# Kernel optimization log

Measured on AMD Instinct MI355X. Metric: run time of the kernel, lower is better.

Reference implementation:

```python
import jax, jax.numpy as jnp
import numpy as np

B, C, H, W = 8, 64, 128, 128
OC, KH, KW = 64, 3, 3
STRIDE, PAD, DIL = 1, 1, 1
DG = 1            # deformable groups
G = 1             # conv groups
K = KH * KW
HO = (H + 2 * PAD - DIL * (KH - 1) - 1) // STRIDE + 1
WO = (W + 2 * PAD - DIL * (KW - 1) - 1) // STRIDE + 1


def setup_inputs() -> dict:
    key = jax.random.key(0)
    k1, k2, k3, k4 = jax.random.split(key, 4)
    input_tensor = jax.random.normal(k1, (B, C, H, W), dtype=jnp.float32)
    offset = jax.random.normal(k2, (B, DG * 2 * K, HO, WO), dtype=jnp.float32)
    mask = jax.random.uniform(k3, (B, DG * K, HO, WO), dtype=jnp.float32)
    n = C * KH * KW
    std_v = 1.0 / np.sqrt(n)
    weight = jax.random.uniform(k4, (OC, C // G, KH, KW), dtype=jnp.float32,
                                minval=-std_v, maxval=std_v)
    bias = jnp.zeros((OC,), dtype=jnp.float32)
    return {"input_tensor": input_tensor, "offset": offset, "mask": mask,
            "weight": weight, "bias": bias}


def _bilinear_sample(img, py, px):
    # img: [Cg, H, W]; py, px: [K, HO, WO] fractional sample coords
    y0 = jnp.floor(py).astype(jnp.int32)
    x0 = jnp.floor(px).astype(jnp.int32)
    y1, x1 = y0 + 1, x0 + 1
    wy1 = py - y0.astype(py.dtype)
    wx1 = px - x0.astype(px.dtype)
    wy0, wx0 = 1.0 - wy1, 1.0 - wx1

    def gather(yy, xx):
        valid = ((yy >= 0) & (yy < H) & (xx >= 0) & (xx < W)).astype(img.dtype)
        yc = jnp.clip(yy, 0, H - 1)
        xc = jnp.clip(xx, 0, W - 1)
        return img[:, yc, xc] * valid  # [Cg, K, HO, WO], zero outside

    return (gather(y0, x0) * (wy0 * wx0) + gather(y0, x1) * (wy0 * wx1)
            + gather(y1, x0) * (wy1 * wx0) + gather(y1, x1) * (wy1 * wx1))


def _mdconv(input_tensor, offset, mask, weight, bias):
    Cg = C // DG
    ky = (jnp.arange(K) // KW).astype(jnp.float32)   # kernel row per tap
    kx = (jnp.arange(K) % KW).astype(jnp.float32)    # kernel col per tap
    oy = jnp.arange(HO, dtype=jnp.float32) * STRIDE - PAD
    ox = jnp.arange(WO, dtype=jnp.float32) * STRIDE - PAD
    base_y = ky[:, None] * DIL + oy[None, :]         # [K, HO]
    base_x = kx[:, None] * DIL + ox[None, :]         # [K, WO]

    off = offset.reshape(B, DG, K, 2, HO, WO)
    py = base_y[None, None, :, :, None] + off[:, :, :, 0]  # [B, DG, K, HO, WO]
    px = base_x[None, None, :, None, :] + off[:, :, :, 1]

    imgs = input_tensor.reshape(B, DG, Cg, H, W)
    sample = jax.vmap(jax.vmap(_bilinear_sample))           # over B then DG
    cols = sample(imgs, py, px)                             # [B, DG, Cg, K, HO, WO]
    cols = cols * mask.reshape(B, DG, 1, K, HO, WO)
    cols = cols.reshape(B, G, C // G, K, HO, WO)

    w = weight.reshape(G, OC // G, C // G, K)
    out = jnp.einsum('gock,bgckpq->bgopq', w, cols)
    out = out.reshape(B, OC, HO, WO) + bias[None, :, None, None]
    return out


def reference(input_tensor, offset, mask, weight, bias):
    return _mdconv(input_tensor, offset, mask, weight, bias)
```

## Files before the change

### kernel.cpp

```cpp
#include <hip/hip_runtime.h>
#include <stdint.h>

typedef unsigned short u16;

#define B_ 8
#define C_ 64
#define H_ 128
#define W_ 128
#define OC_ 64
#define HO_ 128
#define WO_ 128
#define HWC_ (H_*W_*C_)
#define PADW 72

typedef __attribute__((ext_vector_type(8))) _Float16 f16x8;
typedef __attribute__((ext_vector_type(2))) _Float16 h2;
typedef __attribute__((ext_vector_type(4))) float f32x4;

__device__ __forceinline__ u16 f2h(float f) {
  union { _Float16 h; u16 u; } c; c.h = (_Float16)f; return c.u;
}
__device__ __forceinline__ uint32_t pkh2(float f) {
  union { _Float16 h[2]; uint32_t u; } c;
  const _Float16 h = (_Float16)f;
  c.h[0] = h; c.h[1] = h; return c.u;
}

__global__ void wprep_kernel(const float* __restrict__ w, u16* __restrict__ wk2) {
  const int idx = blockIdx.x * 256 + threadIdx.x;
  const int j    = idx & 7;
  const int lane = (idx >> 3) & 63;
  const int kk   = (idx >> 9) & 1;
  const int m    = (idx >> 10) & 1;
  const int wr   = (idx >> 11) & 1;
  const int k    = idx >> 12;
  const int oc = wr*32 + m*16 + (lane & 15);
  const int c  = kk*32 + (lane >> 4)*8 + j;
  wk2[idx] = f2h(w[(oc*C_ + c)*9 + k]);
}

__global__ __launch_bounds__(256) void nhwc_kernel(const float* __restrict__ in,
                                                   u16* __restrict__ nhwc) {
  __shared__ float t[64][65];
  const int b = blockIdx.z, h = blockIdx.y, w0 = blockIdx.x * 64;
  const int tid = threadIdx.x;
  for (int idx = tid; idx < 64*64; idx += 256) {
    int c = idx >> 6, w = idx & 63;
    t[w][c] = in[((b*C_ + c)*H_ + h)*W_ + w0 + w];
  }
  __syncthreads();
  for (int idx = tid; idx < 64*64; idx += 256) {
    int w = idx >> 6, c = idx & 63;
    nhwc[((b*H_ + h)*W_ + w0 + w)*C_ + c] = f2h(t[w][c]);
  }
}

__device__ __forceinline__ uint32_t blendh(uint32_t g00, uint32_t g01,
                                           uint32_t g10, uint32_t g11, uint4 w) {
  h2 s = __builtin_bit_cast(h2, g00) * __builtin_bit_cast(h2, w.x)
       + __builtin_bit_cast(h2, g01) * __builtin_bit_cast(h2, w.y)
       + __builtin_bit_cast(h2, g10) * __builtin_bit_cast(h2, w.z)
       + __builtin_bit_cast(h2, g11) * __builtin_bit_cast(h2, w.w);
  return __builtin_bit_cast(uint32_t, s);
}

__global__ __launch_bounds__(128, 8) void mdconv_main(
    const float* __restrict__ offs, const float* __restrict__ mask,
    const float* __restrict__ bias, const u16* __restrict__ nhwc,
    const u16* __restrict__ wk2, float* __restrict__ out)
{
  __shared__ u16 clds[32*PADW];
  __shared__ int2 pA[288];
  __shared__ uint4 pW[288];

  const int tid = threadIdx.x;
  const int lane = tid & 63;
  const int wv = tid >> 6;
  const int b = blockIdx.z;
  const int p = blockIdx.y;
  const int q0 = blockIdx.x * 32;

  for (int item = tid; item < 288; item += 128) {
    const int k = item >> 5;
    const int px = item & 31;
    const int q = q0 + px;
    const int ky = k / 3, kx = k % 3;
    const float oy = offs[((b*18 + 2*k)*HO_ + p)*WO_ + q];
    const float ox = offs[((b*18 + 2*k + 1)*HO_ + p)*WO_ + q];
    const float mm = mask[((b*9 + k)*HO_ + p)*WO_ + q];
    const float py  = (float)(ky + p - 1) + oy;
    const float pxx = (float)(kx + q - 1) + ox;
    const float y0f = floorf(py), x0f = floorf(pxx);
    const int y0 = (int)y0f, x0 = (int)x0f;
    const int y1 = y0 + 1, x1 = x0 + 1;
    const float wy1 = py - y0f, wx1 = pxx - x0f;
    const float wy0 = 1.f - wy1, wx0 = 1.f - wx1;
    const bool vy0 = (y0 >= 0) & (y0 < H_);
    const bool vy1 = (y1 >= 0) & (y1 < H_);
    const bool vx0 = (x0 >= 0) & (x0 < W_);
    const bool vx1 = (x1 >= 0) & (x1 < W_);
    const float w00 = (vy0 & vx0) ? wy0*wx0*mm : 0.f;
    const float w01 = (vy0 & vx1) ? wy0*wx1*mm : 0.f;
    const float w10 = (vy1 & vx0) ? wy1*wx0*mm : 0.f;
    const float w11 = (vy1 & vx1) ? wy1*wx1*mm : 0.f;
    const int y0c = min(max(y0,0),H_-1), y1c = min(max(y1,0),H_-1);
    const int x0c = min(max(x0,0),W_-1), x1c = min(max(x1,0),W_-1);
    const int dx = (x1c - x0c) * C_;
    const int dy = (y1c - y0c) * W_ * C_;
    pA[item] = make_int2(b*HWC_ + (y0c*W_ + x0c)*C_, dx | (dy << 16));
    pW[item] = make_uint4(pkh2(w00), pkh2(w01), pkh2(w10), pkh2(w11));
  }
  __syncthreads();

  f32x4 acc00 = {0.f,0.f,0.f,0.f};
  f32x4 acc01 = acc00, acc10 = acc00, acc11 = acc00;
  const int wr = wv;
  const int px0 = tid >> 3;
  const int c8 = (tid & 7) * 8;

  for (int k = 0; k < 9; ++k) {
    const u16* wg = wk2 + (k*2 + wr)*2048 + lane*8;
    const f16x8 a00 = *(const f16x8*)(wg);
    const f16x8 a01 = *(const f16x8*)(wg + 512);
    const f16x8 a10 = *(const f16x8*)(wg + 1024);
    const f16x8 a11 = *(const f16x8*)(wg + 1536);

    {
      const int piA = k*32 + px0, piB = piA + 16;
      const int2 aA = pA[piA];
      const int2 aB = pA[piB];
      const uint4 wA = pW[piA];
      const uint4 wB = pW[piB];
      const u16* sA = nhwc + aA.x + c8;
      const u16* sB = nhwc + aB.x + c8;
      const int dxA = aA.y & 0xFFFF, dyA = ((uint32_t)aA.y) >> 16;
      const int dxB = aB.y & 0xFFFF, dyB = ((uint32_t)aB.y) >> 16;
      const uint4 gA00 = *(const uint4*)(sA);
      const uint4 gA01 = *(const uint4*)(sA + dxA);
      const uint4 gA10 = *(const uint4*)(sA + dyA);
      const uint4 gA11 = *(const uint4*)(sA + dyA + dxA);
      const uint4 gB00 = *(const uint4*)(sB);
      const uint4 gB01 = *(const uint4*)(sB + dxB);
      const uint4 gB10 = *(const uint4*)(sB + dyB);
      const uint4 gB11 = *(const uint4*)(sB + dyB + dxB);
      uint4 rA, rB;
      rA.x = blendh(gA00.x, gA01.x, gA10.x, gA11.x, wA);
      rA.y = blendh(gA00.y, gA01.y, gA10.y, gA11.y, wA);
      rA.z = blendh(gA00.z, gA01.z, gA10.z, gA11.z, wA);
      rA.w = blendh(gA00.w, gA01.w, gA10.w, gA11.w, wA);
      rB.x = blendh(gB00.x, gB01.x, gB10.x, gB11.x, wB);
      rB.y = blendh(gB00.y, gB01.y, gB10.y, gB11.y, wB);
      rB.z = blendh(gB00.z, gB01.z, gB10.z, gB11.z, wB);
      rB.w = blendh(gB00.w, gB01.w, gB10.w, gB11.w, wB);
      *(uint4*)(&clds[px0*PADW + c8]) = rA;
      *(uint4*)(&clds[(px0+16)*PADW + c8]) = rB;
    }
    __syncthreads();

    const u16* cb = &clds[(lane & 15)*PADW + (lane >> 4)*8];
    const f16x8 b00 = *(const f16x8*)(cb);
    const f16x8 b01 = *(const f16x8*)(cb + 32);
    const f16x8 b10 = *(const f16x8*)(cb + 16*PADW);
    const f16x8 b11 = *(const f16x8*)(cb + 16*PADW + 32);
    acc00 = __builtin_amdgcn_mfma_f32_16x16x32_f16(a00, b00, acc00, 0, 0, 0);
    acc00 = __builtin_amdgcn_mfma_f32_16x16x32_f16(a01, b01, acc00, 0, 0, 0);
    acc01 = __builtin_amdgcn_mfma_f32_16x16x32_f16(a00, b10, acc01, 0, 0, 0);
    acc01 = __builtin_amdgcn_mfma_f32_16x16x32_f16(a01, b11, acc01, 0, 0, 0);
    acc10 = __builtin_amdgcn_mfma_f32_16x16x32_f16(a10, b00, acc10, 0, 0, 0);
    acc10 = __builtin_amdgcn_mfma_f32_16x16x32_f16(a11, b01, acc10, 0, 0, 0);
    acc11 = __builtin_amdgcn_mfma_f32_16x16x32_f16(a10, b10, acc11, 0, 0, 0);
    acc11 = __builtin_amdgcn_mfma_f32_16x16x32_f16(a11, b11, acc11, 0, 0, 0);
    if (k < 8) __syncthreads();
  }

  const int qc = q0 + (lane & 15);
  const int ocr = wr*32 + (lane >> 4)*4;
  #pragma unroll
  for (int m = 0; m < 2; ++m) {
    #pragma unroll
    for (int n = 0; n < 2; ++n) {
      const f32x4 a = (m==0) ? (n==0 ? acc00 : acc01) : (n==0 ? acc10 : acc11);
      #pragma unroll
      for (int j = 0; j < 4; ++j) {
        const int oc = ocr + m*16 + j;
        out[((b*OC_ + oc)*HO_ + p)*WO_ + qc + n*16] = a[j] + bias[oc];
      }
    }
  }
}

extern "C" void kernel_launch(void* const* d_in, const int* in_sizes, int n_in,
                              void* d_out, int out_size, void* d_ws, size_t ws_size,
                              hipStream_t stream) {
  const float* input  = (const float*)d_in[0];
  const float* offset = (const float*)d_in[1];
  const float* mask   = (const float*)d_in[2];
  const float* weight = (const float*)d_in[3];
  const float* bias   = (const float*)d_in[4];
  float* out = (float*)d_out;

  u16* nhwc = (u16*)d_ws;
  u16* wk2  = nhwc + (size_t)B_*H_*W_*C_;

  hipLaunchKernelGGL(wprep_kernel, dim3(144), dim3(256), 0, stream, weight, wk2);
  hipLaunchKernelGGL(nhwc_kernel, dim3(2, 128, 8), dim3(256), 0, stream, input, nhwc);
  hipLaunchKernelGGL(mdconv_main, dim3(4, 128, 8), dim3(128), 0, stream,
                     offset, mask, bias, nhwc, wk2, out);
}
```

Baseline: 55.62 us.

## Process two kernel taps per barrier with double-buffered LDS and swizzle block order

The im2col staging buffer is doubled so two taps are gathered and blended before a single barrier, then both are consumed by MFMAs. This halves the number of __syncthreads per block and exposes more independent global gathers per round. The grid is flattened to 1D and remapped with an XCD-style swizzle (id&7), so consecutive blocks on the same XCD cover a batch's neighbouring rows for L2 locality. Launch bounds are relaxed from 8 to 4 blocks per CU, which allows more registers but may lower occupancy.

```diff
diff --git a/kernel.cpp b/kernel.cpp
--- a/kernel.cpp
+++ b/kernel.cpp
@@ -64,21 +64,23 @@
   return __builtin_bit_cast(uint32_t, s);
 }
 
-__global__ __launch_bounds__(128, 8) void mdconv_main(
+__global__ __launch_bounds__(128, 4) void mdconv_main(
     const float* __restrict__ offs, const float* __restrict__ mask,
     const float* __restrict__ bias, const u16* __restrict__ nhwc,
     const u16* __restrict__ wk2, float* __restrict__ out)
 {
-  __shared__ u16 clds[32*PADW];
+  __shared__ u16 clds[2][32*PADW];
   __shared__ int2 pA[288];
   __shared__ uint4 pW[288];
 
   const int tid = threadIdx.x;
   const int lane = tid & 63;
   const int wv = tid >> 6;
-  const int b = blockIdx.z;
-  const int p = blockIdx.y;
-  const int q0 = blockIdx.x * 32;
+  const uint32_t id = blockIdx.x;
+  const uint32_t sid = (id & 7) * 512 + (id >> 3);
+  const int b  = sid >> 9;
+  const int p  = (sid >> 2) & 127;
+  const int q0 = (sid & 3) * 32;
 
   for (int item = tid; item < 288; item += 128) {
     const int k = item >> 5;
@@ -118,60 +120,66 @@
   const int px0 = tid >> 3;
   const int c8 = (tid & 7) * 8;
 
-  for (int k = 0; k < 9; ++k) {
-    const u16* wg = wk2 + (k*2 + wr)*2048 + lane*8;
-    const f16x8 a00 = *(const f16x8*)(wg);
-    const f16x8 a01 = *(const f16x8*)(wg + 512);
-    const f16x8 a10 = *(const f16x8*)(wg + 1024);
-    const f16x8 a11 = *(const f16x8*)(wg + 1536);
-
-    {
-      const int piA = k*32 + px0, piB = piA + 16;
-      const int2 aA = pA[piA];
-      const int2 aB = pA[piB];
-      const uint4 wA = pW[piA];
-      const uint4 wB = pW[piB];
-      const u16* sA = nhwc + aA.x + c8;
-      const u16* sB = nhwc + aB.x + c8;
-      const int dxA = aA.y & 0xFFFF, dyA = ((uint32_t)aA.y) >> 16;
-      const int dxB = aB.y & 0xFFFF, dyB = ((uint32_t)aB.y) >> 16;
-      const uint4 gA00 = *(const uint4*)(sA);
-      const uint4 gA01 = *(const uint4*)(sA + dxA);
-      const uint4 gA10 = *(const uint4*)(sA + dyA);
-      const uint4 gA11 = *(const uint4*)(sA + dyA + dxA);
-      const uint4 gB00 = *(const uint4*)(sB);
-      const uint4 gB01 = *(const uint4*)(sB + dxB);
-      const uint4 gB10 = *(const uint4*)(sB + dyB);
-      const uint4 gB11 = *(const uint4*)(sB + dyB + dxB);
-      uint4 rA, rB;
-      rA.x = blendh(gA00.x, gA01.x, gA10.x, gA11.x, wA);
-      rA.y = blendh(gA00.y, gA01.y, gA10.y, gA11.y, wA);
-      rA.z = blendh(gA00.z, gA01.z, gA10.z, gA11.z, wA);
-      rA.w = blendh(gA00.w, gA01.w, gA10.w, gA11.w, wA);
-      rB.x = blendh(gB00.x, gB01.x, gB10.x, gB11.x, wB);
-      rB.y = blendh(gB00.y, gB01.y, gB10.y, gB11.y, wB);
-      rB.z = blendh(gB00.z, gB01.z, gB10.z, gB11.z, wB);
-      rB.w = blendh(gB00.w, gB01.w, gB10.w, gB11.w, wB);
-      *(uint4*)(&clds[px0*PADW + c8]) = rA;
-      *(uint4*)(&clds[(px0+16)*PADW + c8]) = rB;
-    }
+#define COLB(k_, buf_) { \
+    const int piA = (k_)*32 + px0, piB = piA + 16; \
+    const int2 aA = pA[piA]; const int2 aB = pA[piB]; \
+    const uint4 wA = pW[piA]; const uint4 wB = pW[piB]; \
+    const u16* sA = nhwc + aA.x + c8; \
+    const u16* sB = nhwc + aB.x + c8; \
+    const int dxA = aA.y & 0xFFFF, dyA = ((uint32_t)aA.y) >> 16; \
+    const int dxB = aB.y & 0xFFFF, dyB = ((uint32_t)aB.y) >> 16; \
+    const uint4 gA00 = *(const uint4*)(sA); \
+    const uint4 gA01 = *(const uint4*)(sA + dxA); \
+    const uint4 gA10 = *(const uint4*)(sA + dyA); \
+    const uint4 gA11 = *(const uint4*)(sA + dyA + dxA); \
+    const uint4 gB00 = *(const uint4*)(sB); \
+    const uint4 gB01 = *(const uint4*)(sB + dxB); \
+    const uint4 gB10 = *(const uint4*)(sB + dyB); \
+    const uint4 gB11 = *(const uint4*)(sB + dyB + dxB); \
+    uint4 rA, rB; \
+    rA.x = blendh(gA00.x, gA01.x, gA10.x, gA11.x, wA); \
+    rA.y = blendh(gA00.y, gA01.y, gA10.y, gA11.y, wA); \
+    rA.z = blendh(gA00.z, gA01.z, gA10.z, gA11.z, wA); \
+    rA.w = blendh(gA00.w, gA01.w, gA10.w, gA11.w, wA); \
+    rB.x = blendh(gB00.x, gB01.x, gB10.x, gB11.x, wB); \
+    rB.y = blendh(gB00.y, gB01.y, gB10.y, gB11.y, wB); \
+    rB.z = blendh(gB00.z, gB01.z, gB10.z, gB11.z, wB); \
+    rB.w = blendh(gB00.w, gB01.w, gB10.w, gB11.w, wB); \
+    *(uint4*)(&clds[buf_][px0*PADW + c8]) = rA; \
+    *(uint4*)(&clds[buf_][(px0+16)*PADW + c8]) = rB; }
+
+#define MFMA8(k_, buf_) { \
+    const u16* wg = wk2 + ((k_)*2 + wr)*2048 + lane*8; \
+    const f16x8 a00 = *(const f16x8*)(wg); \
+    const f16x8 a01 = *(const f16x8*)(wg + 512); \
+    const f16x8 a10 = *(const f16x8*)(wg + 1024); \
+    const f16x8 a11 = *(const f16x8*)(wg + 1536); \
+    const u16* cb = &clds[buf_][(lane & 15)*PADW + (lane >> 4)*8]; \
+    const f16x8 b00 = *(const f16x8*)(cb); \
+    const f16x8 b01 = *(const f16x8*)(cb + 32); \
+    const f16x8 b10 = *(const f16x8*)(cb + 16*PADW); \
+    const f16x8 b11 = *(const f16x8*)(cb + 16*PADW + 32); \
+    acc00 = __builtin_amdgcn_mfma_f32_16x16x32_f16(a00, b00, acc00, 0, 0, 0); \
+    acc00 = __builtin_amdgcn_mfma_f32_16x16x32_f16(a01, b01, acc00, 0, 0, 0); \
+    acc01 = __builtin_amdgcn_mfma_f32_16x16x32_f16(a00, b10, acc01, 0, 0, 0); \
+    acc01 = __builtin_amdgcn_mfma_f32_16x16x32_f16(a01, b11, acc01, 0, 0, 0); \
+    acc10 = __builtin_amdgcn_mfma_f32_16x16x32_f16(a10, b00, acc10, 0, 0, 0); \
+    acc10 = __builtin_amdgcn_mfma_f32_16x16x32_f16(a11, b01, acc10, 0, 0, 0); \
+    acc11 = __builtin_amdgcn_mfma_f32_16x16x32_f16(a10, b10, acc11, 0, 0, 0); \
+    acc11 = __builtin_amdgcn_mfma_f32_16x16x32_f16(a11, b11, acc11, 0, 0, 0); }
+
+  for (int r = 0; r < 4; ++r) {
+    const int k0 = 2*r;
+    COLB(k0, 0);
+    COLB(k0 + 1, 1);
     __syncthreads();
-
-    const u16* cb = &clds[(lane & 15)*PADW + (lane >> 4)*8];
-    const f16x8 b00 = *(const f16x8*)(cb);
-    const f16x8 b01 = *(const f16x8*)(cb + 32);
-    const f16x8 b10 = *(const f16x8*)(cb + 16*PADW);
-    const f16x8 b11 = *(const f16x8*)(cb + 16*PADW + 32);
-    acc00 = __builtin_amdgcn_mfma_f32_16x16x32_f16(a00, b00, acc00, 0, 0, 0);
-    acc00 = __builtin_amdgcn_mfma_f32_16x16x32_f16(a01, b01, acc00, 0, 0, 0);
-    acc01 = __builtin_amdgcn_mfma_f32_16x16x32_f16(a00, b10, acc01, 0, 0, 0);
-    acc01 = __builtin_amdgcn_mfma_f32_16x16x32_f16(a01, b11, acc01, 0, 0, 0);
-    acc10 = __builtin_amdgcn_mfma_f32_16x16x32_f16(a10, b00, acc10, 0, 0, 0);
-    acc10 = __builtin_amdgcn_mfma_f32_16x16x32_f16(a11, b01, acc10, 0, 0, 0);
-    acc11 = __builtin_amdgcn_mfma_f32_16x16x32_f16(a10, b10, acc11, 0, 0, 0);
-    acc11 = __builtin_amdgcn_mfma_f32_16x16x32_f16(a11, b11, acc11, 0, 0, 0);
-    if (k < 8) __syncthreads();
-  }
+    MFMA8(k0, 0);
+    MFMA8(k0 + 1, 1);
+    __syncthreads();
+  }
+  COLB(8, 0);
+  __syncthreads();
+  MFMA8(8, 0);
 
   const int qc = q0 + (lane & 15);
   const int ocr = wr*32 + (lane >> 4)*4;
@@ -204,6 +212,6 @@
 
   hipLaunchKernelGGL(wprep_kernel, dim3(144), dim3(256), 0, stream, weight, wk2);
   hipLaunchKernelGGL(nhwc_kernel, dim3(2, 128, 8), dim3(256), 0, stream, input, nhwc);
-  hipLaunchKernelGGL(mdconv_main, dim3(4, 128, 8), dim3(128), 0, stream,
+  hipLaunchKernelGGL(mdconv_main, dim3(4096), dim3(128), 0, stream,
                      offset, mask, bias, nhwc, wk2, out);
 }
```

Result: no change. 55.43 us (-0.3%).
